# Kernel optimization log

Hardware: AMD Instinct MI355X
Metric: run time of the kernel (lower is better)

The kernel has to match this reference:

```python
import jax, jax.numpy as jnp
import numpy as np

N_ITEMS = 100000
N_INTENTS = 512
H = 128
ALPHA = 0.5
TOPK = 3  # torch code: sim.topk(3, 1)


def _leaky_relu(x):
    return jnp.where(x > 0, x, 0.2 * x)  # nn.LeakyReLU(0.2)


def setup_inputs() -> dict:
    key = jax.random.key(0)
    k0, k1, k2, k3, k4, k5 = jax.random.split(key, 6)
    s = 1.0 / np.sqrt(H)
    return {
        "item_emb": jax.random.normal(k0, (N_ITEMS, H), jnp.float32),
        "intent_emb": jax.random.normal(k1, (N_INTENTS, H), jnp.float32),
        "Wq": (jax.random.normal(k2, (H, H), jnp.float32) * s),  # lq.weight
        "Wk": (jax.random.normal(k3, (H, H), jnp.float32) * s),  # lk.weight
        "wa": (jax.random.normal(k4, (H,), jnp.float32) * s),    # la.weight (1,H)
        "wb": (jax.random.normal(k5, (H,), jnp.float32) * s),    # lb.weight (1,H)
        "n_items": N_ITEMS,
        "n_intents": N_INTENTS,
    }


def reference(item_emb, intent_emb, Wq, Wk, wa, wb, n_items, n_intents):
    h = item_emb.shape[1]
    # dense similarity + row softmax + top-3 sparsification (indices only matter downstream)
    sim = (item_emb @ Wq.T) @ (intent_emb @ Wk.T).T / jnp.sqrt(jnp.float32(h))
    sim = jax.nn.softmax(sim, axis=1)                      # [n_items, n_intents]
    _, topi = jax.lax.top_k(sim, TOPK)                     # [n_items, 3]
    edge_item = jnp.repeat(jnp.arange(n_items), TOPK)      # [E]
    edge_intent = topi.reshape(-1)                         # [E]

    # --- GNNCell ---
    # att1: edges oriented intent<-item, softmax per intent row (segment softmax)
    s1 = _leaky_relu((intent_emb[edge_intent] * item_emb[edge_item]) @ wa)  # [E]
    m1 = jax.ops.segment_max(s1, edge_intent, num_segments=n_intents)
    e1 = jnp.exp(s1 - m1[edge_intent])
    d1 = jax.ops.segment_sum(e1, edge_intent, num_segments=n_intents)
    w1 = e1 / d1[edge_intent]
    intent_new = jax.ops.segment_sum(w1[:, None] * item_emb[edge_item],
                                     edge_intent, num_segments=n_intents)  # [n_intents, H]

    # att2: edges oriented item<-intent; each item has exactly 3 edges -> softmax over axis 1
    s2 = _leaky_relu((item_emb[edge_item] * intent_new[edge_intent]) @ wb)
    w2 = jax.nn.softmax(s2.reshape(n_items, TOPK), axis=1)  # [n_items, 3]
    item_nei = jnp.einsum("nk,nkh->nh", w2, intent_new[topi])

    return ALPHA * item_emb + (1.0 - ALPHA) * item_nei
```

## Files before the change

kernel.cpp:

```cpp
#include <hip/hip_runtime.h>
#include <math.h>

#define N_ITEMS 100000
#define N_INT   512
#define H       128
#define IPW     8
#define IPB     32
#define TILE    512
#define MAXTILES 2048

typedef unsigned int u32;

__device__ __forceinline__ float wave_sum(float v) {
#pragma unroll
  for (int d = 1; d < 64; d <<= 1) v += __shfl_xor(v, d, 64);
  return v;
}

__global__ void k_projK(const float* __restrict__ intent, const float* __restrict__ Wk,
                        float* __restrict__ K) {
  __shared__ float row[H];
  int j = blockIdx.x, h = threadIdx.x;
  row[h] = intent[j * H + h];
  __syncthreads();
  float acc = 0.f;
#pragma unroll 8
  for (int k = 0; k < H; ++k) acc += row[k] * Wk[h * H + k];
  K[j * H + h] = acc;
}

__global__ void k_projM(const float* __restrict__ Wq, const float* __restrict__ K,
                        float* __restrict__ M) {
  __shared__ float row[H];
  int j = blockIdx.x, k = threadIdx.x;
  row[k] = K[j * H + k];
  __syncthreads();
  float acc = 0.f;
#pragma unroll 8
  for (int a = 0; a < H; ++a) acc += Wq[a * H + k] * row[a];
  M[k * N_INT + j] = acc * 0.08838834764831845f;
}

__global__ __launch_bounds__(256, 3) void k_simtop(
    const float* __restrict__ item, const float* __restrict__ M,
    const float* __restrict__ intent, const float* __restrict__ wa,
    int* __restrict__ topi, float* __restrict__ s1buf, int* __restrict__ counts) {
  const int tid = threadIdx.x;
  const int lane = tid & 63;
  const int wv = __builtin_amdgcn_readfirstlane(tid >> 6);
  const int ibase = blockIdx.x * IPB + wv * IPW;

  float acc[IPW][8];
#pragma unroll
  for (int i = 0; i < IPW; ++i)
#pragma unroll
    for (int jj = 0; jj < 8; ++jj) acc[i][jj] = 0.f;

  const float* mlane = M + 4 * lane;
#pragma unroll 2
  for (int k4 = 0; k4 < H / 4; ++k4) {
    float4 av[IPW];
#pragma unroll
    for (int i = 0; i < IPW; ++i)
      av[i] = *reinterpret_cast<const float4*>(item + (size_t)(ibase + i) * H + k4 * 4);
#pragma unroll
    for (int kk = 0; kk < 4; ++kk) {
      const float* rp = mlane + (k4 * 4 + kk) * N_INT;
      float4 m0 = *reinterpret_cast<const float4*>(rp);
      float4 m1 = *reinterpret_cast<const float4*>(rp + 256);
#pragma unroll
      for (int i = 0; i < IPW; ++i) {
        float a = (kk == 0) ? av[i].x : (kk == 1) ? av[i].y : (kk == 2) ? av[i].z : av[i].w;
        acc[i][0] += a * m0.x; acc[i][1] += a * m0.y;
        acc[i][2] += a * m0.z; acc[i][3] += a * m0.w;
        acc[i][4] += a * m1.x; acc[i][5] += a * m1.y;
        acc[i][6] += a * m1.z; acc[i][7] += a * m1.w;
      }
    }
  }

  const float wal = wa[lane], wah = wa[64 + lane];
#pragma unroll
  for (int i = 0; i < IPW; ++i) {
    float tv0 = -INFINITY, tv1 = -INFINITY, tv2 = -INFINITY;
    int ti0 = 0x7fffffff, ti1 = 0x7fffffff, ti2 = 0x7fffffff;
    auto push = [&](float v, int j) {
      bool b2 = (v > tv2) || (v == tv2 && j < ti2);
      if (b2) {
        bool b1 = (v > tv1) || (v == tv1 && j < ti1);
        if (b1) {
          bool b0 = (v > tv0) || (v == tv0 && j < ti0);
          if (b0) { tv2 = tv1; ti2 = ti1; tv1 = tv0; ti1 = ti0; tv0 = v; ti0 = j; }
          else    { tv2 = tv1; ti2 = ti1; tv1 = v; ti1 = j; }
        } else    { tv2 = v; ti2 = j; }
      }
    };
#pragma unroll
    for (int jj = 0; jj < 8; ++jj) {
      int j = (jj < 4) ? (4 * lane + jj) : (256 + 4 * lane + (jj - 4));
      push(acc[i][jj], j);
    }
#pragma unroll
    for (int d = 1; d < 64; d <<= 1) {
      float ov0 = __shfl_xor(tv0, d, 64), ov1 = __shfl_xor(tv1, d, 64), ov2 = __shfl_xor(tv2, d, 64);
      int   oi0 = __shfl_xor(ti0, d, 64), oi1 = __shfl_xor(ti1, d, 64), oi2 = __shfl_xor(ti2, d, 64);
      push(ov0, oi0); push(ov1, oi1); push(ov2, oi2);
    }
    const int gi = ibase + i;
    const float itl = item[(size_t)gi * H + lane], ith = item[(size_t)gi * H + 64 + lane];
    const float pl = itl * wal, ph = ith * wah;
    float s0 = pl * intent[ti0 * H + lane] + ph * intent[ti0 * H + 64 + lane];
    float s1 = pl * intent[ti1 * H + lane] + ph * intent[ti1 * H + 64 + lane];
    float s2 = pl * intent[ti2 * H + lane] + ph * intent[ti2 * H + 64 + lane];
#pragma unroll
    for (int d = 1; d < 64; d <<= 1) {
      float t0 = __shfl_xor(s0, d, 64);
      float t1 = __shfl_xor(s1, d, 64);
      float t2 = __shfl_xor(s2, d, 64);
      s0 += t0; s1 += t1; s2 += t2;
    }
    s0 = (s0 > 0.f) ? s0 : 0.2f * s0;
    s1 = (s1 > 0.f) ? s1 : 0.2f * s1;
    s2 = (s2 > 0.f) ? s2 : 0.2f * s2;
    if (lane == 0) {
      topi[gi * 3 + 0] = ti0; s1buf[gi * 3 + 0] = s0; atomicAdd(&counts[ti0], 1);
      topi[gi * 3 + 1] = ti1; s1buf[gi * 3 + 1] = s1; atomicAdd(&counts[ti1], 1);
      topi[gi * 3 + 2] = ti2; s1buf[gi * 3 + 2] = s2; atomicAdd(&counts[ti2], 1);
    }
  }
}

__global__ void k_scan(const int* __restrict__ counts, int* __restrict__ offs,
                       int* __restrict__ cursor, int* __restrict__ descs,
                       int* __restrict__ ntl) {
  __shared__ int s[N_INT];
  __shared__ int base;
  int t = threadIdx.x;
  if (t == 0) base = 0;
  int c = counts[t];
  s[t] = c;
  __syncthreads();
  for (int off = 1; off < N_INT; off <<= 1) {
    int v = (t >= off) ? s[t - off] : 0;
    __syncthreads();
    s[t] += v;
    __syncthreads();
  }
  int excl = s[t] - c;
  offs[t] = excl;
  cursor[t] = excl;
  if (t == N_INT - 1) offs[N_INT] = s[t];
  int nt = (c + TILE - 1) / TILE;
  int my = atomicAdd(&base, nt);
  for (int k = 0; k < nt; ++k) {
    descs[2 * (my + k)] = t;
    descs[2 * (my + k) + 1] = excl + k * TILE;
  }
  __syncthreads();
  if (t == 0) ntl[0] = base;
}

__global__ void k_scatter(const int* __restrict__ topi, const float* __restrict__ s1buf,
                          int* __restrict__ cursor, int* __restrict__ eitem,
                          float* __restrict__ es1) {
  int gi = blockIdx.x * 256 + threadIdx.x;
  if (gi >= N_ITEMS) return;
#pragma unroll
  for (int e = 0; e < 3; ++e) {
    int j = topi[gi * 3 + e];
    int pos = atomicAdd(&cursor[j], 1);
    eitem[pos] = gi;
    es1[pos] = s1buf[gi * 3 + e];
  }
}

__global__ __launch_bounds__(256) void k_agg(
    const float* __restrict__ item, const int* __restrict__ offs,
    const int* __restrict__ descs, const int* __restrict__ ntl,
    const int* __restrict__ eitem, const float* __restrict__ es1,
    float* __restrict__ num, float* __restrict__ denom) {
  int bt = blockIdx.x;
  if (bt >= ntl[0]) return;
  int j = descs[2 * bt];
  int beg = descs[2 * bt + 1];
  int end = min(offs[j + 1], beg + TILE);
  __shared__ float red[256];
  __shared__ float rd[2];
  int t = threadIdx.x;
  int h = t & 127, sub = t >> 7;
  float acc = 0.f, dp = 0.f;
  const float* ip = item + h;
#pragma unroll 4
  for (int e = beg + sub; e < end; e += 2) {
    float e1 = expf(es1[e]);
    acc += e1 * ip[(size_t)eitem[e] * H];
    dp += e1;
  }
  red[t] = acc;
  if (h == 0) rd[sub] = dp;
  __syncthreads();
  if (t < 128) atomicAdd(&num[j * H + t], red[t] + red[t + 128]);
  if (t == 0) atomicAdd(&denom[j], rd[0] + rd[1]);
}

__global__ __launch_bounds__(256) void k_final(
    const float* __restrict__ item, const int* __restrict__ topi,
    const float* __restrict__ num, const float* __restrict__ denom,
    const float* __restrict__ wb, float* __restrict__ out) {
  int tid = threadIdx.x;
  int lane = tid & 63;
  int wv = __builtin_amdgcn_readfirstlane(tid >> 6);
  int gi = blockIdx.x * 4 + wv;
  const float il = item[(size_t)gi * H + lane], ih = item[(size_t)gi * H + 64 + lane];
  const float wbl = wb[lane], wbh = wb[64 + lane];
  int j0 = topi[gi * 3 + 0], j1 = topi[gi * 3 + 1], j2 = topi[gi * 3 + 2];
  float d0 = denom[j0], d1 = denom[j1], d2 = denom[j2];
  float r0 = d0 > 0.f ? 1.f / d0 : 0.f;
  float r1 = d1 > 0.f ? 1.f / d1 : 0.f;
  float r2 = d2 > 0.f ? 1.f / d2 : 0.f;
  float n0l = num[j0 * H + lane] * r0, n0h = num[j0 * H + 64 + lane] * r0;
  float n1l = num[j1 * H + lane] * r1, n1h = num[j1 * H + 64 + lane] * r1;
  float n2l = num[j2 * H + lane] * r2, n2h = num[j2 * H + 64 + lane] * r2;
  float s0 = wave_sum(il * n0l * wbl + ih * n0h * wbh);
  float s1 = wave_sum(il * n1l * wbl + ih * n1h * wbh);
  float s2 = wave_sum(il * n2l * wbl + ih * n2h * wbh);
  s0 = s0 > 0.f ? s0 : 0.2f * s0;
  s1 = s1 > 0.f ? s1 : 0.2f * s1;
  s2 = s2 > 0.f ? s2 : 0.2f * s2;
  float mx = fmaxf(s0, fmaxf(s1, s2));
  float e0 = expf(s0 - mx), e1 = expf(s1 - mx), e2 = expf(s2 - mx);
  float inv = 1.f / (e0 + e1 + e2);
  float w0 = e0 * inv, w1 = e1 * inv, w2 = e2 * inv;
  out[(size_t)gi * H + lane]      = 0.5f * il + 0.5f * (w0 * n0l + w1 * n1l + w2 * n2l);
  out[(size_t)gi * H + 64 + lane] = 0.5f * ih + 0.5f * (w0 * n0h + w1 * n1h + w2 * n2h);
}

extern "C" void kernel_launch(void* const* d_in, const int* in_sizes, int n_in,
                              void* d_out, int out_size, void* d_ws, size_t ws_size,
                              hipStream_t stream) {
  (void)in_sizes; (void)n_in; (void)out_size; (void)ws_size;
  const float* item   = (const float*)d_in[0];
  const float* intent = (const float*)d_in[1];
  const float* Wq     = (const float*)d_in[2];
  const float* Wk     = (const float*)d_in[3];
  const float* wa     = (const float*)d_in[4];
  const float* wb     = (const float*)d_in[5];
  float* out = (float*)d_out;

  char* w = (char*)d_ws;
  auto alloc = [&](size_t bytes) {
    char* p = w;
    w += (bytes + 255) & ~(size_t)255;
    return p;
  };
  float* K      = (float*)alloc(N_INT * H * 4);
  float* M      = (float*)alloc((size_t)H * N_INT * 4);
  int*   topi   = (int*)alloc((size_t)N_ITEMS * 3 * 4);
  float* s1b    = (float*)alloc((size_t)N_ITEMS * 3 * 4);
  int*   offs   = (int*)alloc((N_INT + 1) * 4);
  int*   cursor = (int*)alloc(N_INT * 4);
  int*   eitem  = (int*)alloc((size_t)N_ITEMS * 3 * 4);
  float* es1    = (float*)alloc((size_t)N_ITEMS * 3 * 4);
  int*   descs  = (int*)alloc(MAXTILES * 2 * 4);
  char*  zbase  = w;
  int*   counts = (int*)alloc(N_INT * 4);
  int*   ntl    = (int*)alloc(4);
  float* denom  = (float*)alloc(N_INT * 4);
  float* num    = (float*)alloc(N_INT * H * 4);
  size_t zlen   = (size_t)(w - zbase);

  hipMemsetAsync(zbase, 0, zlen, stream);
  k_projK<<<N_INT, H, 0, stream>>>(intent, Wk, K);
  k_projM<<<N_INT, H, 0, stream>>>(Wq, K, M);
  k_simtop<<<N_ITEMS / IPB, 256, 0, stream>>>(item, M, intent, wa, topi, s1b, counts);
  k_scan<<<1, N_INT, 0, stream>>>(counts, offs, cursor, descs, ntl);
  k_scatter<<<(N_ITEMS + 255) / 256, 256, 0, stream>>>(topi, s1b, cursor, eitem, es1);
  k_agg<<<MAXTILES, 256, 0, stream>>>(item, offs, descs, ntl, eitem, es1, num, denom);
  k_final<<<N_ITEMS / 4, 256, 0, stream>>>(item, topi, num, denom, wb, out);
}
```

Baseline: 818.6 us.

## Restructure sim/top-3 kernel into 64-intent chunks with LDS transpose for top-k

Measured after the change: 1.150 ms. +40.4%, slower.

```diff
diff --git a/kernel.cpp b/kernel.cpp
--- a/kernel.cpp
+++ b/kernel.cpp
@@ -41,92 +41,108 @@
   M[k * N_INT + j] = acc * 0.08838834764831845f;
 }
 
-__global__ __launch_bounds__(256, 3) void k_simtop(
+__global__ __launch_bounds__(256) void k_simtop(
     const float* __restrict__ item, const float* __restrict__ M,
     const float* __restrict__ intent, const float* __restrict__ wa,
     int* __restrict__ topi, float* __restrict__ s1buf, int* __restrict__ counts) {
+  __shared__ float xch[4][IPW * 68];
   const int tid = threadIdx.x;
   const int lane = tid & 63;
   const int wv = __builtin_amdgcn_readfirstlane(tid >> 6);
-  const int ibase = blockIdx.x * IPB + wv * IPW;
-
-  float acc[IPW][8];
-#pragma unroll
-  for (int i = 0; i < IPW; ++i)
-#pragma unroll
-    for (int jj = 0; jj < 8; ++jj) acc[i][jj] = 0.f;
-
-  const float* mlane = M + 4 * lane;
+  const int ibase = __builtin_amdgcn_readfirstlane(blockIdx.x * IPB + wv * IPW);
+  float* xc = &xch[wv][0];
+  const int g = lane >> 3;
+  const int o = lane & 7;
+
+  auto push3 = [](float v, int j, float& t0, float& t1, float& t2,
+                  int& i0, int& i1, int& i2) {
+    bool b2 = (v > t2) || (v == t2 && j < i2);
+    if (b2) {
+      bool b1 = (v > t1) || (v == t1 && j < i1);
+      if (b1) {
+        bool b0 = (v > t0) || (v == t0 && j < i0);
+        if (b0) { t2 = t1; i2 = i1; t1 = t0; i1 = i0; t0 = v; i0 = j; }
+        else    { t2 = t1; i2 = i1; t1 = v; i1 = j; }
+      } else    { t2 = v; i2 = j; }
+    }
+  };
+
+  float rv0 = -INFINITY, rv1 = -INFINITY, rv2 = -INFINITY;
+  int ri0 = 0x7fffffff, ri1 = 0x7fffffff, ri2 = 0x7fffffff;
+
+#pragma unroll 1
+  for (int jb = 0; jb < 8; ++jb) {
+    float acc[IPW];
+#pragma unroll
+    for (int i = 0; i < IPW; ++i) acc[i] = 0.f;
+    const float* mp = M + jb * 64 + lane;
 #pragma unroll 2
-  for (int k4 = 0; k4 < H / 4; ++k4) {
-    float4 av[IPW];
-#pragma unroll
-    for (int i = 0; i < IPW; ++i)
-      av[i] = *reinterpret_cast<const float4*>(item + (size_t)(ibase + i) * H + k4 * 4);
-#pragma unroll
-    for (int kk = 0; kk < 4; ++kk) {
-      const float* rp = mlane + (k4 * 4 + kk) * N_INT;
-      float4 m0 = *reinterpret_cast<const float4*>(rp);
-      float4 m1 = *reinterpret_cast<const float4*>(rp + 256);
-#pragma unroll
-      for (int i = 0; i < IPW; ++i) {
-        float a = (kk == 0) ? av[i].x : (kk == 1) ? av[i].y : (kk == 2) ? av[i].z : av[i].w;
-        acc[i][0] += a * m0.x; acc[i][1] += a * m0.y;
-        acc[i][2] += a * m0.z; acc[i][3] += a * m0.w;
-        acc[i][4] += a * m1.x; acc[i][5] += a * m1.y;
-        acc[i][6] += a * m1.z; acc[i][7] += a * m1.w;
+    for (int k4 = 0; k4 < H / 4; ++k4) {
+      float4 av[IPW];
+#pragma unroll
+      for (int i = 0; i < IPW; ++i)
+        av[i] = *reinterpret_cast<const float4*>(item + (size_t)(ibase + i) * H + k4 * 4);
+#pragma unroll
+      for (int kk = 0; kk < 4; ++kk) {
+        float m = mp[(k4 * 4 + kk) * N_INT];
+#pragma unroll
+        for (int i = 0; i < IPW; ++i) {
+          float a = (kk == 0) ? av[i].x : (kk == 1) ? av[i].y : (kk == 2) ? av[i].z : av[i].w;
+          acc[i] += a * m;
+        }
       }
     }
-  }
-
-  const float wal = wa[lane], wah = wa[64 + lane];
-#pragma unroll
-  for (int i = 0; i < IPW; ++i) {
+#pragma unroll
+    for (int i = 0; i < IPW; ++i) xc[i * 68 + lane] = acc[i];
+    float4 b0 = *reinterpret_cast<const float4*>(xc + g * 68 + o * 8);
+    float4 b1 = *reinterpret_cast<const float4*>(xc + g * 68 + o * 8 + 4);
     float tv0 = -INFINITY, tv1 = -INFINITY, tv2 = -INFINITY;
     int ti0 = 0x7fffffff, ti1 = 0x7fffffff, ti2 = 0x7fffffff;
-    auto push = [&](float v, int j) {
-      bool b2 = (v > tv2) || (v == tv2 && j < ti2);
-      if (b2) {
-        bool b1 = (v > tv1) || (v == tv1 && j < ti1);
-        if (b1) {
-          bool b0 = (v > tv0) || (v == tv0 && j < ti0);
-          if (b0) { tv2 = tv1; ti2 = ti1; tv1 = tv0; ti1 = ti0; tv0 = v; ti0 = j; }
-          else    { tv2 = tv1; ti2 = ti1; tv1 = v; ti1 = j; }
-        } else    { tv2 = v; ti2 = j; }
-      }
-    };
-#pragma unroll
-    for (int jj = 0; jj < 8; ++jj) {
-      int j = (jj < 4) ? (4 * lane + jj) : (256 + 4 * lane + (jj - 4));
-      push(acc[i][jj], j);
-    }
-#pragma unroll
-    for (int d = 1; d < 64; d <<= 1) {
+    float lv[8] = {b0.x, b0.y, b0.z, b0.w, b1.x, b1.y, b1.z, b1.w};
+#pragma unroll
+    for (int t = 0; t < 8; ++t)
+      push3(lv[t], jb * 64 + o * 8 + t, tv0, tv1, tv2, ti0, ti1, ti2);
+#pragma unroll
+    for (int d = 1; d < 8; d <<= 1) {
       float ov0 = __shfl_xor(tv0, d, 64), ov1 = __shfl_xor(tv1, d, 64), ov2 = __shfl_xor(tv2, d, 64);
       int   oi0 = __shfl_xor(ti0, d, 64), oi1 = __shfl_xor(ti1, d, 64), oi2 = __shfl_xor(ti2, d, 64);
-      push(ov0, oi0); push(ov1, oi1); push(ov2, oi2);
+      push3(ov0, oi0, tv0, tv1, tv2, ti0, ti1, ti2);
+      push3(ov1, oi1, tv0, tv1, tv2, ti0, ti1, ti2);
+      push3(ov2, oi2, tv0, tv1, tv2, ti0, ti1, ti2);
     }
-    const int gi = ibase + i;
-    const float itl = item[(size_t)gi * H + lane], ith = item[(size_t)gi * H + 64 + lane];
-    const float pl = itl * wal, ph = ith * wah;
-    float s0 = pl * intent[ti0 * H + lane] + ph * intent[ti0 * H + 64 + lane];
-    float s1 = pl * intent[ti1 * H + lane] + ph * intent[ti1 * H + 64 + lane];
-    float s2 = pl * intent[ti2 * H + lane] + ph * intent[ti2 * H + 64 + lane];
-#pragma unroll
-    for (int d = 1; d < 64; d <<= 1) {
-      float t0 = __shfl_xor(s0, d, 64);
-      float t1 = __shfl_xor(s1, d, 64);
-      float t2 = __shfl_xor(s2, d, 64);
-      s0 += t0; s1 += t1; s2 += t2;
-    }
-    s0 = (s0 > 0.f) ? s0 : 0.2f * s0;
-    s1 = (s1 > 0.f) ? s1 : 0.2f * s1;
-    s2 = (s2 > 0.f) ? s2 : 0.2f * s2;
-    if (lane == 0) {
-      topi[gi * 3 + 0] = ti0; s1buf[gi * 3 + 0] = s0; atomicAdd(&counts[ti0], 1);
-      topi[gi * 3 + 1] = ti1; s1buf[gi * 3 + 1] = s1; atomicAdd(&counts[ti1], 1);
-      topi[gi * 3 + 2] = ti2; s1buf[gi * 3 + 2] = s2; atomicAdd(&counts[ti2], 1);
-    }
+    push3(tv0, ti0, rv0, rv1, rv2, ri0, ri1, ri2);
+    push3(tv1, ti1, rv0, rv1, rv2, ri0, ri1, ri2);
+    push3(tv2, ti2, rv0, rv1, rv2, ri0, ri1, ri2);
+  }
+
+  const int gi = ibase + g;
+  float s0 = 0.f, s1 = 0.f, s2 = 0.f;
+#pragma unroll
+  for (int c = 0; c < 4; ++c) {
+    int hoff = o * 16 + c * 4;
+    float4 it = *reinterpret_cast<const float4*>(item + (size_t)gi * H + hoff);
+    float4 w4 = *reinterpret_cast<const float4*>(wa + hoff);
+    float4 p  = make_float4(it.x * w4.x, it.y * w4.y, it.z * w4.z, it.w * w4.w);
+    float4 i0 = *reinterpret_cast<const float4*>(intent + (size_t)ri0 * H + hoff);
+    float4 i1 = *reinterpret_cast<const float4*>(intent + (size_t)ri1 * H + hoff);
+    float4 i2 = *reinterpret_cast<const float4*>(intent + (size_t)ri2 * H + hoff);
+    s0 += p.x * i0.x + p.y * i0.y + p.z * i0.z + p.w * i0.w;
+    s1 += p.x * i1.x + p.y * i1.y + p.z * i1.z + p.w * i1.w;
+    s2 += p.x * i2.x + p.y * i2.y + p.z * i2.z + p.w * i2.w;
+  }
+#pragma unroll
+  for (int d = 1; d < 8; d <<= 1) {
+    s0 += __shfl_xor(s0, d, 64);
+    s1 += __shfl_xor(s1, d, 64);
+    s2 += __shfl_xor(s2, d, 64);
+  }
+  s0 = (s0 > 0.f) ? s0 : 0.2f * s0;
+  s1 = (s1 > 0.f) ? s1 : 0.2f * s1;
+  s2 = (s2 > 0.f) ? s2 : 0.2f * s2;
+  if (o == 0) {
+    topi[gi * 3 + 0] = ri0; s1buf[gi * 3 + 0] = s0; atomicAdd(&counts[ri0], 1);
+    topi[gi * 3 + 1] = ri1; s1buf[gi * 3 + 1] = s1; atomicAdd(&counts[ri1], 1);
+    topi[gi * 3 + 2] = ri2; s1buf[gi * 3 + 2] = s2; atomicAdd(&counts[ri2], 1);
   }
 }
 
```

## Stage item tile in LDS and split intents across wave halves in simtop

Applied to the files above, without the earlier changes.

New measurement: 1.398 ms. +70.8%, slower.

```diff
diff --git a/kernel.cpp b/kernel.cpp
--- a/kernel.cpp
+++ b/kernel.cpp
@@ -4,8 +4,8 @@
 #define N_ITEMS 100000
 #define N_INT   512
 #define H       128
+#define IPB     32
 #define IPW     8
-#define IPB     32
 #define TILE    512
 #define MAXTILES 2048
 
@@ -15,6 +15,19 @@
 #pragma unroll
   for (int d = 1; d < 64; d <<= 1) v += __shfl_xor(v, d, 64);
   return v;
+}
+
+__device__ __forceinline__ void push3(float v, int j, float& t0, float& t1, float& t2,
+                                      int& i0, int& i1, int& i2) {
+  bool b2 = (v > t2) || (v == t2 && j < i2);
+  if (b2) {
+    bool b1 = (v > t1) || (v == t1 && j < i1);
+    if (b1) {
+      bool b0 = (v > t0) || (v == t0 && j < i0);
+      if (b0) { t2 = t1; i2 = i1; t1 = t0; i1 = i0; t0 = v; i0 = j; }
+      else    { t2 = t1; i2 = i1; t1 = v; i1 = j; }
+    } else    { t2 = v; i2 = j; }
+  }
 }
 
 __global__ void k_projK(const float* __restrict__ intent, const float* __restrict__ Wk,
@@ -41,91 +54,102 @@
   M[k * N_INT + j] = acc * 0.08838834764831845f;
 }
 
-__global__ __launch_bounds__(256, 3) void k_simtop(
+__global__ __launch_bounds__(512) void k_simtop(
     const float* __restrict__ item, const float* __restrict__ M,
     const float* __restrict__ intent, const float* __restrict__ wa,
     int* __restrict__ topi, float* __restrict__ s1buf, int* __restrict__ counts) {
+  __shared__ float sit[IPB * H];
+  __shared__ float mv[IPB][6];
+  __shared__ int   mi[IPB][6];
   const int tid = threadIdx.x;
   const int lane = tid & 63;
   const int wv = __builtin_amdgcn_readfirstlane(tid >> 6);
-  const int ibase = blockIdx.x * IPB + wv * IPW;
-
-  float acc[IPW][8];
+  const int ig = (wv & 3) * IPW;
+  const int half = wv >> 2;
+  const int jh = half * 256;
+
+#pragma unroll
+  for (int r = 0; r < 2; ++r) {
+    __builtin_amdgcn_global_load_lds(
+        (const __attribute__((address_space(1))) u32*)(item + (size_t)blockIdx.x * (IPB * H) + r * 2048 + tid * 4),
+        (__attribute__((address_space(3))) u32*)(sit + r * 2048 + wv * 256), 16, 0, 0);
+  }
+  __syncthreads();
+
+  float acc[IPW][4];
 #pragma unroll
   for (int i = 0; i < IPW; ++i)
 #pragma unroll
-    for (int jj = 0; jj < 8; ++jj) acc[i][jj] = 0.f;
-
-  const float* mlane = M + 4 * lane;
-#pragma unroll 2
-  for (int k4 = 0; k4 < H / 4; ++k4) {
-    float4 av[IPW];
-#pragma unroll
-    for (int i = 0; i < IPW; ++i)
-      av[i] = *reinterpret_cast<const float4*>(item + (size_t)(ibase + i) * H + k4 * 4);
-#pragma unroll
-    for (int kk = 0; kk < 4; ++kk) {
-      const float* rp = mlane + (k4 * 4 + kk) * N_INT;
-      float4 m0 = *reinterpret_cast<const float4*>(rp);
-      float4 m1 = *reinterpret_cast<const float4*>(rp + 256);
-#pragma unroll
-      for (int i = 0; i < IPW; ++i) {
-        float a = (kk == 0) ? av[i].x : (kk == 1) ? av[i].y : (kk == 2) ? av[i].z : av[i].w;
-        acc[i][0] += a * m0.x; acc[i][1] += a * m0.y;
-        acc[i][2] += a * m0.z; acc[i][3] += a * m0.w;
-        acc[i][4] += a * m1.x; acc[i][5] += a * m1.y;
-        acc[i][6] += a * m1.z; acc[i][7] += a * m1.w;
-      }
+    for (int jj = 0; jj < 4; ++jj) acc[i][jj] = 0.f;
+
+  const float* mp = M + jh + 4 * lane;
+#pragma unroll 4
+  for (int k = 0; k < H; ++k) {
+    float4 m = *reinterpret_cast<const float4*>(mp + (size_t)k * N_INT);
+#pragma unroll
+    for (int i = 0; i < IPW; ++i) {
+      float a = sit[(ig + i) * H + k];
+      acc[i][0] += a * m.x; acc[i][1] += a * m.y;
+      acc[i][2] += a * m.z; acc[i][3] += a * m.w;
     }
   }
 
-  const float wal = wa[lane], wah = wa[64 + lane];
 #pragma unroll
   for (int i = 0; i < IPW; ++i) {
     float tv0 = -INFINITY, tv1 = -INFINITY, tv2 = -INFINITY;
     int ti0 = 0x7fffffff, ti1 = 0x7fffffff, ti2 = 0x7fffffff;
-    auto push = [&](float v, int j) {
-      bool b2 = (v > tv2) || (v == tv2 && j < ti2);
-      if (b2) {
-        bool b1 = (v > tv1) || (v == tv1 && j < ti1);
-        if (b1) {
-          bool b0 = (v > tv0) || (v == tv0 && j < ti0);
-          if (b0) { tv2 = tv1; ti2 = ti1; tv1 = tv0; ti1 = ti0; tv0 = v; ti0 = j; }
-          else    { tv2 = tv1; ti2 = ti1; tv1 = v; ti1 = j; }
-        } else    { tv2 = v; ti2 = j; }
-      }
-    };
-#pragma unroll
-    for (int jj = 0; jj < 8; ++jj) {
-      int j = (jj < 4) ? (4 * lane + jj) : (256 + 4 * lane + (jj - 4));
-      push(acc[i][jj], j);
-    }
+    const int jb = jh + 4 * lane;
+    push3(acc[i][0], jb + 0, tv0, tv1, tv2, ti0, ti1, ti2);
+    push3(acc[i][1], jb + 1, tv0, tv1, tv2, ti0, ti1, ti2);
+    push3(acc[i][2], jb + 2, tv0, tv1, tv2, ti0, ti1, ti2);
+    push3(acc[i][3], jb + 3, tv0, tv1, tv2, ti0, ti1, ti2);
 #pragma unroll
     for (int d = 1; d < 64; d <<= 1) {
       float ov0 = __shfl_xor(tv0, d, 64), ov1 = __shfl_xor(tv1, d, 64), ov2 = __shfl_xor(tv2, d, 64);
       int   oi0 = __shfl_xor(ti0, d, 64), oi1 = __shfl_xor(ti1, d, 64), oi2 = __shfl_xor(ti2, d, 64);
-      push(ov0, oi0); push(ov1, oi1); push(ov2, oi2);
+      push3(ov0, oi0, tv0, tv1, tv2, ti0, ti1, ti2);
+      push3(ov1, oi1, tv0, tv1, tv2, ti0, ti1, ti2);
+      push3(ov2, oi2, tv0, tv1, tv2, ti0, ti1, ti2);
     }
-    const int gi = ibase + i;
-    const float itl = item[(size_t)gi * H + lane], ith = item[(size_t)gi * H + 64 + lane];
-    const float pl = itl * wal, ph = ith * wah;
-    float s0 = pl * intent[ti0 * H + lane] + ph * intent[ti0 * H + 64 + lane];
-    float s1 = pl * intent[ti1 * H + lane] + ph * intent[ti1 * H + 64 + lane];
-    float s2 = pl * intent[ti2 * H + lane] + ph * intent[ti2 * H + 64 + lane];
-#pragma unroll
-    for (int d = 1; d < 64; d <<= 1) {
-      float t0 = __shfl_xor(s0, d, 64);
-      float t1 = __shfl_xor(s1, d, 64);
-      float t2 = __shfl_xor(s2, d, 64);
-      s0 += t0; s1 += t1; s2 += t2;
+    if (lane == 0) {
+      mv[ig + i][half * 3 + 0] = tv0; mi[ig + i][half * 3 + 0] = ti0;
+      mv[ig + i][half * 3 + 1] = tv1; mi[ig + i][half * 3 + 1] = ti1;
+      mv[ig + i][half * 3 + 2] = tv2; mi[ig + i][half * 3 + 2] = ti2;
     }
-    s0 = (s0 > 0.f) ? s0 : 0.2f * s0;
-    s1 = (s1 > 0.f) ? s1 : 0.2f * s1;
-    s2 = (s2 > 0.f) ? s2 : 0.2f * s2;
-    if (lane == 0) {
-      topi[gi * 3 + 0] = ti0; s1buf[gi * 3 + 0] = s0; atomicAdd(&counts[ti0], 1);
-      topi[gi * 3 + 1] = ti1; s1buf[gi * 3 + 1] = s1; atomicAdd(&counts[ti1], 1);
-      topi[gi * 3 + 2] = ti2; s1buf[gi * 3 + 2] = s2; atomicAdd(&counts[ti2], 1);
+  }
+  __syncthreads();
+
+  if (half == 0) {
+    const float wal = wa[lane], wah = wa[64 + lane];
+#pragma unroll
+    for (int i = 0; i < IPW; ++i) {
+      const int it = ig + i;
+      float v0 = -INFINITY, v1 = -INFINITY, v2 = -INFINITY;
+      int j0 = 0x7fffffff, j1 = 0x7fffffff, j2 = 0x7fffffff;
+#pragma unroll
+      for (int c = 0; c < 6; ++c)
+        push3(mv[it][c], mi[it][c], v0, v1, v2, j0, j1, j2);
+      const int gi = blockIdx.x * IPB + it;
+      const float itl = sit[it * H + lane], ith = sit[it * H + 64 + lane];
+      const float pl = itl * wal, ph = ith * wah;
+      float s0 = pl * intent[(size_t)j0 * H + lane] + ph * intent[(size_t)j0 * H + 64 + lane];
+      float s1 = pl * intent[(size_t)j1 * H + lane] + ph * intent[(size_t)j1 * H + 64 + lane];
+      float s2 = pl * intent[(size_t)j2 * H + lane] + ph * intent[(size_t)j2 * H + 64 + lane];
+#pragma unroll
+      for (int d = 1; d < 64; d <<= 1) {
+        float t0 = __shfl_xor(s0, d, 64);
+        float t1 = __shfl_xor(s1, d, 64);
+        float t2 = __shfl_xor(s2, d, 64);
+        s0 += t0; s1 += t1; s2 += t2;
+      }
+      s0 = (s0 > 0.f) ? s0 : 0.2f * s0;
+      s1 = (s1 > 0.f) ? s1 : 0.2f * s1;
+      s2 = (s2 > 0.f) ? s2 : 0.2f * s2;
+      if (lane == 0) {
+        topi[gi * 3 + 0] = j0; s1buf[gi * 3 + 0] = s0; atomicAdd(&counts[j0], 1);
+        topi[gi * 3 + 1] = j1; s1buf[gi * 3 + 1] = s1; atomicAdd(&counts[j1], 1);
+        topi[gi * 3 + 2] = j2; s1buf[gi * 3 + 2] = s2; atomicAdd(&counts[j2], 1);
+      }
     }
   }
 }
@@ -272,7 +296,7 @@
   hipMemsetAsync(zbase, 0, zlen, stream);
   k_projK<<<N_INT, H, 0, stream>>>(intent, Wk, K);
   k_projM<<<N_INT, H, 0, stream>>>(Wq, K, M);
-  k_simtop<<<N_ITEMS / IPB, 256, 0, stream>>>(item, M, intent, wa, topi, s1b, counts);
+  k_simtop<<<N_ITEMS / IPB, 512, 0, stream>>>(item, M, intent, wa, topi, s1b, counts);
   k_scan<<<1, N_INT, 0, stream>>>(counts, offs, cursor, descs, ntl);
   k_scatter<<<(N_ITEMS + 255) / 256, 256, 0, stream>>>(topi, s1b, cursor, eitem, es1);
   k_agg<<<MAXTILES, 256, 0, stream>>>(item, offs, descs, ntl, eitem, es1, num, denom);
```
